# Optimization experiments

Hardware: AMD Instinct MI355X
Metric: run time of the kernel (lower is better)

## Reference

```python
import jax, jax.numpy as jnp
import numpy as np
from jax import lax

NEG = -1.0e9


def setup_inputs() -> dict:
    key = jax.random.key(0)
    ks = jax.random.split(key, 12)
    B, S, d, H = 4, 1024, 1024, 16
    sc = 1.0 / np.sqrt(d)
    inp = {
        "query": jax.random.normal(ks[0], (B, S, d), jnp.float32),
        "key": jax.random.normal(ks[1], (B, S, d), jnp.float32),
        "value": jax.random.normal(ks[2], (B, S, d), jnp.float32),
        # causal mask: True = masked (future positions)
        "mask": jnp.triu(jnp.ones((S, S), bool), k=1)[None, None],
        "Wq": jax.random.normal(ks[3], (d, d), jnp.float32) * sc,
        "bq": jnp.zeros((d,), jnp.float32),
        "Wk": jax.random.normal(ks[4], (d, d), jnp.float32) * sc,
        "bk": jnp.zeros((d,), jnp.float32),
        "Wv": jax.random.normal(ks[5], (d, d), jnp.float32) * sc,
        "bv": jnp.zeros((d,), jnp.float32),
        "Wo": jax.random.normal(ks[6], (d, d), jnp.float32) * sc,
        "bo": jnp.zeros((d,), jnp.float32),
        "gammas": jax.random.uniform(ks[7], (H, 1, 1), jnp.float32, -0.05, 0.05),
    }
    return inp


def reference(query, key, value, mask, Wq, bq, Wk, bk, Wv, bv, Wo, bo, gammas):
    B, S, d = query.shape
    H = gammas.shape[0]
    dk = d // H

    def proj(x, W, b):
        # [B,S,d] -> [B,H,S,dk]
        return (x @ W.T + b).reshape(B, S, H, dk).transpose(0, 2, 1, 3)

    q = proj(query, Wq, bq)
    k = proj(key, Wk, bk)
    v = proj(value, Wv, bv)

    scores = jnp.einsum("bhqd,bhkd->bhqk", q, k) / np.float32(np.sqrt(dk))

    # --- distance-decay effect (no-grad block in torch) ---
    p = jax.nn.softmax(jnp.where(mask, NEG, scores), axis=-1)
    distcum = jnp.cumsum(p, axis=-1)
    disttot = jnp.sum(p, axis=-1, keepdims=True)
    idx = jnp.arange(S, dtype=scores.dtype)
    pos = jnp.abs(idx[:, None] - idx[None, :])[None, None]  # [1,1,S,S]
    dist = jnp.sqrt(jnp.clip((disttot - distcum) * pos, 0.0))
    dist = lax.stop_gradient(dist)

    gamma = -jnp.abs(gammas)[None]  # [1,H,1,1]
    total_effect = jnp.clip(jnp.exp(dist * gamma), 1e-5, 1e5)

    gated = jnp.where(mask, NEG, scores * total_effect)
    attn = jax.nn.softmax(gated, axis=-1)
    attn = jnp.where(mask, 0.0, attn)

    out = jnp.einsum("bhqk,bhkd->bhqd", attn, v)
    out = out.transpose(0, 2, 1, 3).reshape(B, S, d)
    out = out @ Wo.T + bo
    return out, attn
```

## Files before the change

### kernel.cpp

```cpp
#include <hip/hip_runtime.h>
#include <hip/hip_bf16.h>

typedef __attribute__((ext_vector_type(8))) short short8;
typedef __attribute__((ext_vector_type(4))) float f32x4;
typedef __attribute__((ext_vector_type(4))) unsigned short us4;

#define MFMA(a, b, c) __builtin_amdgcn_mfma_f32_16x16x32_bf16((a), (b), (c), 0, 0, 0)
#define EXP2(x) __builtin_amdgcn_exp2f(x)

static __device__ inline unsigned short f2b(float f) {
    __hip_bfloat16 h = __float2bfloat16(f);
    return *reinterpret_cast<unsigned short*>(&h);
}
static __device__ inline float b2f(unsigned short u) {
    unsigned int x = ((unsigned int)u) << 16;
    return __builtin_bit_cast(float, x);
}

static __device__ __forceinline__ void gload_lds16(const unsigned short* g, unsigned short* s) {
    __builtin_amdgcn_global_load_lds(
        (const __attribute__((address_space(1))) unsigned int*)(g),
        (__attribute__((address_space(3))) unsigned int*)(s),
        16, 0, 0);
}
#define WAITV(N) asm volatile("s_waitcnt vmcnt(" #N ")" ::: "memory")
#define WAITL    asm volatile("s_waitcnt lgkmcnt(0)" ::: "memory")
#define SBAR     __builtin_amdgcn_s_barrier()
#define SCHED0   __builtin_amdgcn_sched_barrier(0)

__global__ __launch_bounds__(256) void convk(
    const float* __restrict__ i0, const float* __restrict__ i1,
    const float* __restrict__ i2, const float* __restrict__ i3,
    unsigned short* o0, unsigned short* o1, unsigned short* o2, unsigned short* o3, int n)
{
    const float* in; unsigned short* out;
    switch (blockIdx.y) {
        case 0: in = i0; out = o0; break;
        case 1: in = i1; out = o1; break;
        case 2: in = i2; out = o2; break;
        default: in = i3; out = o3; break;
    }
    int i = (blockIdx.x * 256 + threadIdx.x) * 4;
    if (i >= n) return;
    float4 v = *(const float4*)(in + i);
    us4 o;
    o[0] = f2b(v.x); o[1] = f2b(v.y); o[2] = f2b(v.z); o[3] = f2b(v.w);
    *(us4*)(out + i) = o;
}

__global__ __launch_bounds__(256) void gemm_qkv(
    const float* __restrict__ Aq, const float* __restrict__ Ak, const float* __restrict__ Av,
    const unsigned short* __restrict__ wq, const unsigned short* __restrict__ wk,
    const unsigned short* __restrict__ wv,
    const float* __restrict__ bq, const float* __restrict__ bk, const float* __restrict__ bv,
    unsigned short* __restrict__ qh, unsigned short* __restrict__ kh,
    unsigned short* __restrict__ vt,
    int M, int N, int K)
{
    __shared__ unsigned short sA[3][128 * 32];
    __shared__ unsigned short sB[3][128 * 32];

    const int d  = blockIdx.x;
    const int c  = d & 7;
    const int t0 = d >> 3;
    const int nn = t0 & 7;
    const int g  = (t0 >> 3) * 8 + c;
    const int z  = g >> 5;
    const int mm = g & 31;

    const float* A           = z == 0 ? Aq : z == 1 ? Ak : Av;
    const unsigned short* Bm = z == 0 ? wq : z == 1 ? wk : wv;
    const float* bias        = z == 0 ? bq : z == 1 ? bk : bv;
    unsigned short* Cb       = z == 0 ? qh : z == 1 ? kh : vt;
    const int emode          = z == 2 ? 2 : 1;

    const int tid = threadIdx.x;
    const int wave = tid >> 6, lane = tid & 63;
    const int wm = (wave >> 1) * 64, wn = (wave & 1) * 64;
    const int bm = mm * 128, bn = nn * 128;
    const int fr = lane & 15, fg = lane >> 4;

    const int ar = tid >> 1, ac = (tid & 1) * 16;
    const float* Ag = A + (size_t)(bm + ar) * K + ac;
    const unsigned short* Bg = Bm + (size_t)(bn + wave * 32 + (lane >> 2)) * K + (lane & 3) * 8;

    f32x4 acc[4][4] = {};
    const int nt = K >> 5;

    float4 rA[4];
    #define LOAD_A(t)  { const float* p = Ag + ((t) << 5); \
        rA[0] = *(const float4*)(p);     rA[1] = *(const float4*)(p + 4); \
        rA[2] = *(const float4*)(p + 8); rA[3] = *(const float4*)(p + 12); }
    #define GLOAD_B(buf, t) { const unsigned short* p = Bg + ((t) << 5); \
        gload_lds16(p,          &sB[buf][(wave * 32 + 0 ) * 32]); \
        gload_lds16(p + 16 * K, &sB[buf][(wave * 32 + 16) * 32]); }
    #define WRITE_A(buf) { \
        unsigned short* dsts = &sA[buf][ar * 32 + ac]; \
        short8 w; \
        w[0] = (short)f2b(rA[0].x); w[1] = (short)f2b(rA[0].y); \
        w[2] = (short)f2b(rA[0].z); w[3] = (short)f2b(rA[0].w); \
        w[4] = (short)f2b(rA[1].x); w[5] = (short)f2b(rA[1].y); \
        w[6] = (short)f2b(rA[1].z); w[7] = (short)f2b(rA[1].w); \
        *(short8*)(dsts) = w; \
        w[0] = (short)f2b(rA[2].x); w[1] = (short)f2b(rA[2].y); \
        w[2] = (short)f2b(rA[2].z); w[3] = (short)f2b(rA[2].w); \
        w[4] = (short)f2b(rA[3].x); w[5] = (short)f2b(rA[3].y); \
        w[6] = (short)f2b(rA[3].z); w[7] = (short)f2b(rA[3].w); \
        *(short8*)(dsts + 8) = w; }

    LOAD_A(0);
    SCHED0;
    GLOAD_B(0, 0);
    WAITV(2);
    WRITE_A(0);
    LOAD_A(1);
    SCHED0;
    GLOAD_B(1, 1);

    for (int t = 0; t < nt; ++t) {
        const int cur = t % 3;
        if (t + 1 < nt) { WAITV(2); } else { WAITV(0); }
        if (t + 1 < nt) { WRITE_A((t + 1) % 3); }
        if (t + 2 < nt) {
            LOAD_A(t + 2);
            SCHED0;
            GLOAD_B((t + 2) % 3, t + 2);
        }
        WAITL;
        SBAR; SCHED0;

        short8 af[4], bf[4];
        #pragma unroll
        for (int mr = 0; mr < 4; ++mr)
            af[mr] = *(const short8*)&sA[cur][(wm + mr * 16 + fr) * 32 + fg * 8];
        #pragma unroll
        for (int nr = 0; nr < 4; ++nr)
            bf[nr] = *(const short8*)&sB[cur][(wn + nr * 16 + fr) * 32 + fg * 8];
        #pragma unroll
        for (int mr = 0; mr < 4; ++mr)
            #pragma unroll
            for (int nr = 0; nr < 4; ++nr)
                acc[mr][nr] = MFMA(af[mr], bf[nr], acc[mr][nr]);

        SCHED0; SBAR;
    }

    #pragma unroll
    for (int mr = 0; mr < 4; ++mr)
        #pragma unroll
        for (int nr = 0; nr < 4; ++nr)
            #pragma unroll
            for (int j = 0; j < 4; ++j) {
                int m = bm + wm + mr * 16 + fg * 4 + j;
                int n = bn + wn + nr * 16 + fr;
                float v = acc[mr][nr][j] + bias[n];
                int b = m >> 10, s = m & 1023, h = n >> 6, dc = n & 63;
                if (emode == 1)
                    Cb[(((size_t)(b * 16 + h)) * 1024 + s) * 64 + dc] = f2b(v);
                else
                    Cb[(((size_t)(b * 16 + h)) * 64 + dc) * 1024 + s] = f2b(v);
            }
    #undef LOAD_A
    #undef GLOAD_B
    #undef WRITE_A
}

__global__ __launch_bounds__(256) void gemm_wo(
    const unsigned short* __restrict__ A, const unsigned short* __restrict__ Bm,
    const float* __restrict__ bias, float* __restrict__ Cf, int M, int N, int K)
{
    __shared__ unsigned short sA[3][128 * 32];
    __shared__ unsigned short sB[3][128 * 32];

    const int d  = blockIdx.x;
    const int c  = d & 7;
    const int t0 = d >> 3;
    const int nn = t0 & 7;
    const int mm = (t0 >> 3) * 8 + c;

    const int tid = threadIdx.x;
    const int wave = tid >> 6, lane = tid & 63;
    const int wm = (wave >> 1) * 64, wn = (wave & 1) * 64;
    const int bm = mm * 128, bn = nn * 128;
    const int fr = lane & 15, fg = lane >> 4;

    const unsigned short* Ag = A + (size_t)(bm + wave * 32 + (lane >> 2)) * K + (lane & 3) * 8;
    const unsigned short* Bg = Bm + (size_t)(bn + wave * 32 + (lane >> 2)) * K + (lane & 3) * 8;

    #define STAGE(buf, t) { \
        const unsigned short* ap = Ag + ((t) << 5); \
        gload_lds16(ap,          &sA[buf][(wave * 32 + 0 ) * 32]); \
        gload_lds16(ap + 16 * K, &sA[buf][(wave * 32 + 16) * 32]); \
        const unsigned short* bp = Bg + ((t) << 5); \
        gload_lds16(bp,          &sB[buf][(wave * 32 + 0 ) * 32]); \
        gload_lds16(bp + 16 * K, &sB[buf][(wave * 32 + 16) * 32]); }

    f32x4 acc[4][4] = {};
    const int nt = K >> 5;

    STAGE(0, 0); STAGE(1, 1);
    for (int t = 0; t < nt; ++t) {
        const int cur = t % 3;
        if (t + 2 < nt)      { STAGE((t + 2) % 3, t + 2); WAITV(8); }
        else if (t + 1 < nt) { WAITV(4); }
        else                 { WAITV(0); }
        SBAR; SCHED0;

        short8 af[4], bf[4];
        #pragma unroll
        for (int mr = 0; mr < 4; ++mr)
            af[mr] = *(const short8*)&sA[cur][(wm + mr * 16 + fr) * 32 + fg * 8];
        #pragma unroll
        for (int nr = 0; nr < 4; ++nr)
            bf[nr] = *(const short8*)&sB[cur][(wn + nr * 16 + fr) * 32 + fg * 8];
        #pragma unroll
        for (int mr = 0; mr < 4; ++mr)
            #pragma unroll
            for (int nr = 0; nr < 4; ++nr)
                acc[mr][nr] = MFMA(af[mr], bf[nr], acc[mr][nr]);

        SCHED0; SBAR;
    }
    #undef STAGE

    #pragma unroll
    for (int mr = 0; mr < 4; ++mr)
        #pragma unroll
        for (int nr = 0; nr < 4; ++nr)
            #pragma unroll
            for (int j = 0; j < 4; ++j) {
                int m = bm + wm + mr * 16 + fg * 4 + j;
                int n = bn + wn + nr * 16 + fr;
                Cf[(size_t)m * N + n] = acc[mr][nr][j] + bias[n];
            }
}

__global__ __launch_bounds__(256) void attn_fused(
    const unsigned short* __restrict__ Qh,
    const unsigned short* __restrict__ Kh,
    const unsigned short* __restrict__ Vt,
    const float* __restrict__ gammas,
    float* __restrict__ attn_out,
    unsigned short* __restrict__ ctx)
{
    extern __shared__ char smem[];
    const int RS = 1032;
    unsigned short* s_s = (unsigned short*)smem;
    unsigned short* s_q = (unsigned short*)(smem + 16 * RS * 2);
    float* s_inv = (float*)(smem + 16 * RS * 2 + 16 * 72 * 2);
    const int S = 1024;

    int gid = blockIdx.y * gridDim.x + blockIdx.x;
    int jj = gid >> 3;
    const int bh = (gid & 7) * 8 + (jj >> 6);
    const int qb = jj & 63;
    const int q0 = qb * 16;
    const int tid = threadIdx.x;
    const int wave = tid >> 6, lane = tid & 63, fr = lane & 15, fg = lane >> 4;

    {
        int rr = tid >> 4, c4 = (tid & 15) * 4;
        *(uint2*)&s_q[rr * 72 + c4] = *(const uint2*)&Qh[((size_t)bh * S + q0 + rr) * 64 + c4];
    }
    __syncthreads();
    const int kmax = q0 + 15;

    {
        short8 qf0 = *(const short8*)&s_q[fr * 72 + fg * 8];
        short8 qf1 = *(const short8*)&s_q[fr * 72 + 32 + fg * 8];
        const unsigned short* kbase = &Kh[(size_t)bh * S * 64];
        const int iters = (qb >= wave) ? (((qb - wave) >> 2) + 1) : 0;
        #pragma unroll 2
        for (int nf = 0; nf < iters; ++nf) {
            int cb = (nf * 4 + wave) * 16;
            const unsigned short* kb = kbase + (size_t)cb * 64;
            short8 kf0 = *(const short8*)&kb[fr * 64 + fg * 8];
            short8 kf1 = *(const short8*)&kb[fr * 64 + 32 + fg * 8];
            f32x4 a = {0.f, 0.f, 0.f, 0.f};
            a = MFMA(qf0, kf0, a);
            a = MFMA(qf1, kf1, a);
            #pragma unroll
            for (int j = 0; j < 4; ++j)
                s_s[(size_t)(fg * 4 + j) * RS + cb + fr] = f2b(a[j] * 0.18033688f);
        }
    }
    __syncthreads();

    {
        const int r = tid >> 4, sub = tid & 15;
        const int qr = q0 + r;
        unsigned short* srow = &s_s[(size_t)r * RS];
        const float ag2 = fabsf(gammas[bh & 15]) * 1.44269504f;
        const int m = ((qb + 4) >> 2) | 1;
        const int L = 4 * m;
        const int base = sub * L;

        float seg = 0.f;
        for (int c = 0; c < m; ++c) {
            us4 s4 = *(const us4*)&srow[base + c * 4];
            #pragma unroll
            for (int j = 0; j < 4; ++j) {
                int kk = base + c * 4 + j;
                seg += (kk <= qr) ? EXP2(b2f(s4[j])) : 0.f;
            }
        }
        float x = seg, t;
        t = __shfl_up(x, 1, 16); if (sub >= 1) x += t;
        t = __shfl_up(x, 2, 16); if (sub >= 2) x += t;
        t = __shfl_up(x, 4, 16); if (sub >= 4) x += t;
        t = __shfl_up(x, 8, 16); if (sub >= 8) x += t;
        const float T = __shfl(x, 15, 16);
        const float invT = 1.f / T;
        float run = x - seg;

        float ls2 = 0.f;
        for (int c = 0; c < m; ++c) {
            us4 s4 = *(const us4*)&srow[base + c * 4];
            us4 o;
            #pragma unroll
            for (int j = 0; j < 4; ++j) {
                int kk = base + c * 4 + j;
                bool act = kk <= qr;
                float u = b2f(s4[j]);
                float e = act ? EXP2(u) : 0.f;
                run += e;
                float rem = fmaxf(T - run, 0.f) * invT;
                float dist = sqrtf(rem * (float)(qr - kk));
                float te = EXP2(-ag2 * dist);
                float e2 = act ? EXP2(u * te) : 0.f;
                o[j] = f2b(e2);
                ls2 += e2;
            }
            *(us4*)&srow[base + c * 4] = o;
        }
        us4 z = {0, 0, 0, 0};
        for (int c = 4 * L + sub; c < 256; c += 16)
            *(us4*)&srow[c * 4] = z;
        #pragma unroll
        for (int mm = 1; mm < 16; mm <<= 1) ls2 += __shfl_xor(ls2, mm, 16);
        if (sub == 0) s_inv[r] = 1.f / ls2;
    }
    __syncthreads();

    for (int r2 = 0; r2 < 16; ++r2) {
        us4 e4 = *(const us4*)&s_s[(size_t)r2 * RS + tid * 4];
        float iv = s_inv[r2];
        f32x4 w = {b2f(e4[0]) * iv, b2f(e4[1]) * iv, b2f(e4[2]) * iv, b2f(e4[3]) * iv};
        __builtin_nontemporal_store(w,
            (f32x4*)(attn_out + ((size_t)bh * S + q0 + r2) * S + tid * 4));
    }

    {
        const unsigned short* vb = &Vt[(size_t)bh * 64 * S];
        f32x4 acc = {0.f, 0.f, 0.f, 0.f};
        const int ktiles = (kmax + 32) >> 5;
        const unsigned short* prow = &s_s[(size_t)fr * RS];
        #pragma unroll 2
        for (int kt = 0; kt < ktiles; ++kt) {
            short8 pa = *(const short8*)&prow[kt * 32 + fg * 8];
            short8 vf = *(const short8*)&vb[(size_t)(wave * 16 + fr) * S + kt * 32 + fg * 8];
            acc = MFMA(pa, vf, acc);
        }
        int b = bh >> 4, h = bh & 15;
        #pragma unroll
        for (int j = 0; j < 4; ++j) {
            float iv = s_inv[fg * 4 + j];
            ctx[((size_t)b * S + q0 + fg * 4 + j) * 1024 + h * 64 + wave * 16 + fr] = f2b(acc[j] * iv);
        }
    }
}

extern "C" void kernel_launch(void* const* d_in, const int* in_sizes, int n_in,
                              void* d_out, int out_size, void* d_ws, size_t ws_size,
                              hipStream_t stream) {
    const float* query  = (const float*)d_in[0];
    const float* key    = (const float*)d_in[1];
    const float* value  = (const float*)d_in[2];
    const float* Wq = (const float*)d_in[4];
    const float* bq = (const float*)d_in[5];
    const float* Wk = (const float*)d_in[6];
    const float* bk = (const float*)d_in[7];
    const float* Wv = (const float*)d_in[8];
    const float* bv = (const float*)d_in[9];
    const float* Wo = (const float*)d_in[10];
    const float* bo = (const float*)d_in[11];
    const float* gammas = (const float*)d_in[12];

    const int S = 1024, dmodel = 1024;
    const int M = 4 * S;
    const size_t MD = (size_t)M * dmodel;
    const size_t DD = (size_t)dmodel * dmodel;

    char* ws = (char*)d_ws;
    unsigned short* wqb = (unsigned short*)ws;            ws += DD * 2;
    unsigned short* wkb = (unsigned short*)ws;            ws += DD * 2;
    unsigned short* wvb = (unsigned short*)ws;            ws += DD * 2;
    unsigned short* wob = (unsigned short*)ws;            ws += DD * 2;
    unsigned short* qh  = (unsigned short*)ws;            ws += MD * 2;
    unsigned short* kh  = (unsigned short*)ws;            ws += MD * 2;
    unsigned short* vt  = (unsigned short*)ws;            ws += MD * 2;
    unsigned short* ctx = (unsigned short*)ws;            ws += MD * 2;

    float* outp = (float*)d_out;
    float* attn_out = outp + MD;

    convk<<<dim3(1024, 4), 256, 0, stream>>>(Wq, Wk, Wv, Wo, wqb, wkb, wvb, wob, (int)DD);

    gemm_qkv<<<dim3(768), 256, 0, stream>>>(
        query, key, value, wqb, wkb, wvb, bq, bk, bv, qh, kh, vt, M, dmodel, dmodel);

    size_t lds = 16 * 1032 * 2 + 16 * 72 * 2 + 16 * 4;
    attn_fused<<<dim3(64, 64), 256, lds, stream>>>(qh, kh, vt, gammas, attn_out, ctx);

    gemm_wo<<<dim3(256), 256, 0, stream>>>(ctx, wob, bo, outp, M, dmodel, dmodel);
}
```

Before: 175.2 us.

## Pre-convert QKV activations to bf16 and stage both GEMM operands via direct-to-LDS loads

The fp32 query/key/value activations are now converted to bf16 in the existing conversion kernel, which grows to seven inputs. The QKV GEMM then loads both A and B tiles with global_load_lds straight into shared memory, dropping the register-staged fp32 loads, in-loop bf16 conversion and LDS writes. The cost is an extra pass that reads 48MB of fp32 and writes 24MB of bf16, plus three more workspace buffers. The GEMM pipeline becomes simpler, with vmcnt waits only.

```diff
diff --git a/kernel.cpp b/kernel.cpp
--- a/kernel.cpp
+++ b/kernel.cpp
@@ -24,21 +24,26 @@
         16, 0, 0);
 }
 #define WAITV(N) asm volatile("s_waitcnt vmcnt(" #N ")" ::: "memory")
-#define WAITL    asm volatile("s_waitcnt lgkmcnt(0)" ::: "memory")
 #define SBAR     __builtin_amdgcn_s_barrier()
 #define SCHED0   __builtin_amdgcn_sched_barrier(0)
 
 __global__ __launch_bounds__(256) void convk(
-    const float* __restrict__ i0, const float* __restrict__ i1,
-    const float* __restrict__ i2, const float* __restrict__ i3,
-    unsigned short* o0, unsigned short* o1, unsigned short* o2, unsigned short* o3, int n)
+    const float* __restrict__ i0, const float* __restrict__ i1, const float* __restrict__ i2,
+    const float* __restrict__ i3, const float* __restrict__ i4, const float* __restrict__ i5,
+    const float* __restrict__ i6,
+    unsigned short* o0, unsigned short* o1, unsigned short* o2, unsigned short* o3,
+    unsigned short* o4, unsigned short* o5, unsigned short* o6,
+    int nbig, int nsmall)
 {
-    const float* in; unsigned short* out;
+    const float* in; unsigned short* out; int n;
     switch (blockIdx.y) {
-        case 0: in = i0; out = o0; break;
-        case 1: in = i1; out = o1; break;
-        case 2: in = i2; out = o2; break;
-        default: in = i3; out = o3; break;
+        case 0: in = i0; out = o0; n = nbig; break;
+        case 1: in = i1; out = o1; n = nbig; break;
+        case 2: in = i2; out = o2; n = nbig; break;
+        case 3: in = i3; out = o3; n = nsmall; break;
+        case 4: in = i4; out = o4; n = nsmall; break;
+        case 5: in = i5; out = o5; n = nsmall; break;
+        default: in = i6; out = o6; n = nsmall; break;
     }
     int i = (blockIdx.x * 256 + threadIdx.x) * 4;
     if (i >= n) return;
@@ -49,7 +54,8 @@
 }
 
 __global__ __launch_bounds__(256) void gemm_qkv(
-    const float* __restrict__ Aq, const float* __restrict__ Ak, const float* __restrict__ Av,
+    const unsigned short* __restrict__ xq, const unsigned short* __restrict__ xk,
+    const unsigned short* __restrict__ xv,
     const unsigned short* __restrict__ wq, const unsigned short* __restrict__ wk,
     const unsigned short* __restrict__ wv,
     const float* __restrict__ bq, const float* __restrict__ bk, const float* __restrict__ bv,
@@ -68,7 +74,7 @@
     const int z  = g >> 5;
     const int mm = g & 31;
 
-    const float* A           = z == 0 ? Aq : z == 1 ? Ak : Av;
+    const unsigned short* A  = z == 0 ? xq : z == 1 ? xk : xv;
     const unsigned short* Bm = z == 0 ? wq : z == 1 ? wk : wv;
     const float* bias        = z == 0 ? bq : z == 1 ? bk : bv;
     unsigned short* Cb       = z == 0 ? qh : z == 1 ? kh : vt;
@@ -80,53 +86,26 @@
     const int bm = mm * 128, bn = nn * 128;
     const int fr = lane & 15, fg = lane >> 4;
 
-    const int ar = tid >> 1, ac = (tid & 1) * 16;
-    const float* Ag = A + (size_t)(bm + ar) * K + ac;
+    const unsigned short* Ag = A + (size_t)(bm + wave * 32 + (lane >> 2)) * K + (lane & 3) * 8;
     const unsigned short* Bg = Bm + (size_t)(bn + wave * 32 + (lane >> 2)) * K + (lane & 3) * 8;
+
+    #define STAGE(buf, t) { \
+        const unsigned short* ap = Ag + ((t) << 5); \
+        gload_lds16(ap,          &sA[buf][(wave * 32 + 0 ) * 32]); \
+        gload_lds16(ap + 16 * K, &sA[buf][(wave * 32 + 16) * 32]); \
+        const unsigned short* bp = Bg + ((t) << 5); \
+        gload_lds16(bp,          &sB[buf][(wave * 32 + 0 ) * 32]); \
+        gload_lds16(bp + 16 * K, &sB[buf][(wave * 32 + 16) * 32]); }
 
     f32x4 acc[4][4] = {};
     const int nt = K >> 5;
 
-    float4 rA[4];
-    #define LOAD_A(t)  { const float* p = Ag + ((t) << 5); \
-        rA[0] = *(const float4*)(p);     rA[1] = *(const float4*)(p + 4); \
-        rA[2] = *(const float4*)(p + 8); rA[3] = *(const float4*)(p + 12); }
-    #define GLOAD_B(buf, t) { const unsigned short* p = Bg + ((t) << 5); \
-        gload_lds16(p,          &sB[buf][(wave * 32 + 0 ) * 32]); \
-        gload_lds16(p + 16 * K, &sB[buf][(wave * 32 + 16) * 32]); }
-    #define WRITE_A(buf) { \
-        unsigned short* dsts = &sA[buf][ar * 32 + ac]; \
-        short8 w; \
-        w[0] = (short)f2b(rA[0].x); w[1] = (short)f2b(rA[0].y); \
-        w[2] = (short)f2b(rA[0].z); w[3] = (short)f2b(rA[0].w); \
-        w[4] = (short)f2b(rA[1].x); w[5] = (short)f2b(rA[1].y); \
-        w[6] = (short)f2b(rA[1].z); w[7] = (short)f2b(rA[1].w); \
-        *(short8*)(dsts) = w; \
-        w[0] = (short)f2b(rA[2].x); w[1] = (short)f2b(rA[2].y); \
-        w[2] = (short)f2b(rA[2].z); w[3] = (short)f2b(rA[2].w); \
-        w[4] = (short)f2b(rA[3].x); w[5] = (short)f2b(rA[3].y); \
-        w[6] = (short)f2b(rA[3].z); w[7] = (short)f2b(rA[3].w); \
-        *(short8*)(dsts + 8) = w; }
-
-    LOAD_A(0);
-    SCHED0;
-    GLOAD_B(0, 0);
-    WAITV(2);
-    WRITE_A(0);
-    LOAD_A(1);
-    SCHED0;
-    GLOAD_B(1, 1);
-
+    STAGE(0, 0); STAGE(1, 1);
     for (int t = 0; t < nt; ++t) {
         const int cur = t % 3;
-        if (t + 1 < nt) { WAITV(2); } else { WAITV(0); }
-        if (t + 1 < nt) { WRITE_A((t + 1) % 3); }
-        if (t + 2 < nt) {
-            LOAD_A(t + 2);
-            SCHED0;
-            GLOAD_B((t + 2) % 3, t + 2);
-        }
-        WAITL;
+        if (t + 2 < nt)      { STAGE((t + 2) % 3, t + 2); WAITV(8); }
+        else if (t + 1 < nt) { WAITV(4); }
+        else                 { WAITV(0); }
         SBAR; SCHED0;
 
         short8 af[4], bf[4];
@@ -144,6 +123,7 @@
 
         SCHED0; SBAR;
     }
+    #undef STAGE
 
     #pragma unroll
     for (int mr = 0; mr < 4; ++mr)
@@ -160,9 +140,6 @@
                 else
                     Cb[(((size_t)(b * 16 + h)) * 64 + dc) * 1024 + s] = f2b(v);
             }
-    #undef LOAD_A
-    #undef GLOAD_B
-    #undef WRITE_A
 }
 
 __global__ __launch_bounds__(256) void gemm_wo(
@@ -392,6 +369,9 @@
     const size_t DD = (size_t)dmodel * dmodel;
 
     char* ws = (char*)d_ws;
+    unsigned short* xq  = (unsigned short*)ws;            ws += MD * 2;
+    unsigned short* xk  = (unsigned short*)ws;            ws += MD * 2;
+    unsigned short* xv  = (unsigned short*)ws;            ws += MD * 2;
     unsigned short* wqb = (unsigned short*)ws;            ws += DD * 2;
     unsigned short* wkb = (unsigned short*)ws;            ws += DD * 2;
     unsigned short* wvb = (unsigned short*)ws;            ws += DD * 2;
@@ -404,10 +384,12 @@
     float* outp = (float*)d_out;
     float* attn_out = outp + MD;
 
-    convk<<<dim3(1024, 4), 256, 0, stream>>>(Wq, Wk, Wv, Wo, wqb, wkb, wvb, wob, (int)DD);
+    convk<<<dim3(4096, 7), 256, 0, stream>>>(
+        query, key, value, Wq, Wk, Wv, Wo,
+        xq, xk, xv, wqb, wkb, wvb, wob, (int)MD, (int)DD);
 
     gemm_qkv<<<dim3(768), 256, 0, stream>>>(
-        query, key, value, wqb, wkb, wvb, bq, bk, bv, qh, kh, vt, M, dmodel, dmodel);
+        xq, xk, xv, wqb, wkb, wvb, bq, bk, bv, qh, kh, vt, M, dmodel, dmodel);
 
     size_t lds = 16 * 1032 * 2 + 16 * 72 * 2 + 16 * 4;
     attn_fused<<<dim3(64, 64), 256, lds, stream>>>(qh, kh, vt, gammas, attn_out, ctx);
```

After: 179.1 us. 2.3% more time.
